# Kernel tuning notes

Measured on AMD Instinct MI355X. Metric: run time of the kernel, lower is better.

The kernel has to match this reference:

```python
import jax, jax.numpy as jnp
import numpy as np

L_MAX = 119
D_MODEL = 128
N_HEADS = 4
HEAD_DIM = 32


def _rope_tables():
    # matches torch: inv_freq over arange(0,128,2)/128, t=arange(119), cast to bf16
    channel_range = jnp.arange(0, D_MODEL, 2, dtype=jnp.float32)
    inv_freq = 1.0 / (10000.0 ** (channel_range / D_MODEL))
    t = jnp.arange(L_MAX, dtype=jnp.float32)
    freqs = jnp.outer(t, inv_freq)  # (119, 64)
    return jnp.cos(freqs).astype(jnp.bfloat16), jnp.sin(freqs).astype(jnp.bfloat16)


def _apply_rotary(x, cos, sin):
    # x: (b, l, 128); half-rotation on the full model dim (pre head-split)
    l = x.shape[1]
    d = x.shape[-1] // 2
    x1, x2 = x[..., :d], x[..., d:]
    c, s = cos[:l], sin[:l]
    y1 = x1 * c + x2 * s
    y2 = x1 * (-s) + x2 * c
    return jnp.concatenate([y1, y2], axis=-1).astype(x.dtype)


def setup_inputs() -> dict:
    key = jax.random.key(0)
    k1, k2, k3, k4, k5 = jax.random.split(key, 5)
    b, l = 2048, L_MAX
    return {
        "x": jax.random.normal(k1, (b, l, D_MODEL), dtype=jnp.float32),
        "W_qkv": jax.random.normal(k2, (3 * D_MODEL, D_MODEL), dtype=jnp.float32) * 0.05,
        "b_qkv": jax.random.normal(k3, (3 * D_MODEL,), dtype=jnp.float32) * 0.02,
        "W_fc2": jax.random.normal(k4, (D_MODEL, D_MODEL), dtype=jnp.float32) * 0.05,
        "b_fc2": jax.random.normal(k5, (D_MODEL,), dtype=jnp.float32) * 0.02,
    }


def reference(x, W_qkv, b_qkv, W_fc2, b_fc2):
    b, l, _ = x.shape
    cos, sin = _rope_tables()

    qkv = x @ W_qkv.T + b_qkv  # (b, l, 384)
    q, k, v = jnp.split(qkv, 3, axis=-1)
    q = _apply_rotary(q, cos, sin)
    k = _apply_rotary(k, cos, sin)

    # faithful to source: view(b, l, 32, 4) then 'b l d h -> b h l d'
    def split_heads(t):
        return t.reshape(b, l, HEAD_DIM, N_HEADS).transpose(0, 3, 1, 2)  # (b, h, l, d)

    q, k, v = split_heads(q), split_heads(k), split_heads(v)

    scale = 1.0 / np.sqrt(HEAD_DIM)
    scores = jnp.einsum("bhld,bhmd->bhlm", q, k) * scale  # (b, h, l, l)
    causal = jnp.tril(jnp.ones((l, l), dtype=bool))
    scores = jnp.where(causal, scores, jnp.float32(-jnp.inf))
    attn = jax.nn.softmax(scores, axis=-1)
    y = jnp.einsum("bhlm,bhmd->bhld", attn, v)  # (b, h, l, d)

    # faithful to source: transpose(1,2) then view(b, l, 128) -> layout h*32+d
    y = y.transpose(0, 2, 1, 3).reshape(b, l, D_MODEL)
    y = y @ W_fc2.T + b_fc2
    return jax.nn.silu(y)
```

## Files before the change

kernel.cpp:

```cpp
#include <hip/hip_runtime.h>
#include <hip/hip_bf16.h>
#include <math.h>


#define L_SEQ 119
#define D_MODEL 128
#define SCALE 0.17677669529663687f
#define NEGINF -1e30f

typedef __bf16 bf16x8 __attribute__((ext_vector_type(8)));
typedef __bf16 bf16x2 __attribute__((ext_vector_type(2)));
typedef float f32x4 __attribute__((ext_vector_type(4)));

__global__ void rope_tab_kernel(bf16x2* __restrict__ tabb) {
  int i = blockIdx.x * blockDim.x + threadIdx.x;
  if (i >= L_SEQ * 64) return;
  int l = i >> 6, j = i & 63;
  float inv = 1.0f / powf(10000.0f, (float)(2 * j) / 128.0f);
  float f = (float)l * inv;
  bf16x2 cs;
  cs[0] = (__bf16)cosf(f);
  cs[1] = (__bf16)sinf(f);
  tabb[i] = cs;
}

__global__ void wprep_kernel(const float* __restrict__ Wqkv,
                             const float* __restrict__ bqkv,
                             __bf16* __restrict__ Wb, float* __restrict__ bb) {
  int i = blockIdx.x * 256 + threadIdx.x;
  int j = i & 7, lane = (i >> 3) & 63, kb = (i >> 9) & 3, nt = i >> 11;
  int ln15 = lane & 15;
  int nch = nt * 16 + ln15;
  int h = nch / 96, rem = nch % 96, qkv = rem >> 5, d = rem & 31;
  int srow = qkv * 128 + d * 4 + h;
  int k = kb * 32 + (lane >> 4) * 8 + j;
  Wb[i] = (__bf16)Wqkv[srow * 128 + k];
  if (i < 384) {
    int h2 = i / 96, r2 = i % 96, q2 = r2 >> 5, d2 = r2 & 31;
    bb[i] = bqkv[q2 * 128 + d2 * 4 + h2];
  }
}

__global__ void wprep2_kernel(const float* __restrict__ Wfc2,
                              __bf16* __restrict__ Wf2b) {
  int i = blockIdx.x * 256 + threadIdx.x;
  int j = i & 7, lane = (i >> 3) & 63, kb = (i >> 9) & 3, nt = i >> 11;
  int n = nt * 16 + (lane & 15);
  int k = kb * 32 + (lane >> 4) * 8 + j;
  Wf2b[i] = (__bf16)Wfc2[n * 128 + k];
}

__global__ __launch_bounds__(512) void fused_all(
    const float* __restrict__ x, const __bf16* __restrict__ Wb,
    const float* __restrict__ bb, const bf16x2* __restrict__ tabb,
    const __bf16* __restrict__ Wf2b, const float* __restrict__ bfc2,
    float* __restrict__ out) {
  __shared__ __align__(16) __bf16 qs[2 * 119 * 34];
  __shared__ __align__(16) __bf16 ks[2 * 119 * 34];
  __shared__ __align__(16) __bf16 vT[2 * 32 * 128];

  const int t = threadIdx.x, b = blockIdx.x;
  const int lane = t & 63, wv = t >> 6;
  const int ln15 = lane & 15, kg = lane >> 4;
  const int ww = wv & 3, hh = wv >> 2;

  for (int i = t; i < 2 * 32 * 9; i += 512) {
    int hl = i / 288, rem = i % 288, rr = rem / 9, cc = L_SEQ + rem % 9;
    int vr = hl * 32 + rr;
    vT[vr * 128 + (cc ^ ((vr & 7) << 3))] = (__bf16)0.0f;
  }

  for (int g = 0; g < 2; ++g) {
    if (g) __syncthreads();

    bf16x8 af[2][4];
#pragma unroll
    for (int ms = 0; ms < 2; ++ms) {
      int xr = (ww + ms * 4) * 16 + ln15;
      if (xr > L_SEQ - 1) xr = L_SEQ - 1;
      const float* xrow = x + ((size_t)b * L_SEQ + xr) * 128;
#pragma unroll
      for (int kb = 0; kb < 4; ++kb) {
        float4 lo = *(const float4*)&xrow[kb * 32 + kg * 8];
        float4 hi = *(const float4*)&xrow[kb * 32 + kg * 8 + 4];
        bf16x8 v;
        v[0] = (__bf16)lo.x; v[1] = (__bf16)lo.y; v[2] = (__bf16)lo.z; v[3] = (__bf16)lo.w;
        v[4] = (__bf16)hi.x; v[5] = (__bf16)hi.y; v[6] = (__bf16)hi.z; v[7] = (__bf16)hi.w;
        af[ms][kb] = v;
      }
    }

    const int h = 2 * g + hh;
#pragma unroll
    for (int pair = 0; pair < 3; ++pair) {
      f32x4 acc[2][2] = {};
#pragma unroll
      for (int half = 0; half < 2; ++half) {
        const int nt = g * 12 + hh * 6 + pair * 2 + half;
        bf16x8 wf[4];
#pragma unroll
        for (int kb = 0; kb < 4; ++kb)
          wf[kb] = *(const bf16x8*)&Wb[(((nt * 4 + kb) * 64) + lane) * 8];
#pragma unroll
        for (int kb = 0; kb < 4; ++kb) {
          acc[0][half] = __builtin_amdgcn_mfma_f32_16x16x32_bf16(af[0][kb], wf[kb], acc[0][half], 0, 0, 0);
          acc[1][half] = __builtin_amdgcn_mfma_f32_16x16x32_bf16(af[1][kb], wf[kb], acc[1][half], 0, 0, 0);
        }
      }
      const float b0 = bb[(g * 12 + hh * 6 + pair * 2) * 16 + ln15];
      const float b1 = bb[(g * 12 + hh * 6 + pair * 2 + 1) * 16 + ln15];
#pragma unroll
      for (int ms = 0; ms < 2; ++ms) {
        const int mt = ww + ms * 4;
#pragma unroll
        for (int r = 0; r < 4; ++r) {
          int l = mt * 16 + kg * 4 + r;
          if (l < L_SEQ) {
            float v1 = acc[ms][0][r] + b0, v2 = acc[ms][1][r] + b1;
            if (pair < 2) {
              bf16x2 tcs = tabb[l * 64 + 4 * ln15 + h];
              float cs0 = (float)tcs[0], cs1 = (float)tcs[1];
              if (pair == 0) { v1 *= SCALE; v2 *= SCALE; }
              bf16x2 pk;
              pk[0] = (__bf16)(v1 * cs0 + v2 * cs1);
              pk[1] = (__bf16)(v2 * cs0 - v1 * cs1);
              __bf16* base = pair ? ks : qs;
              *(bf16x2*)&base[(hh * L_SEQ + l) * 34 + 2 * ln15] = pk;
            } else {
              int vr0 = hh * 32 + ln15, vr1 = vr0 + 16;
              vT[vr0 * 128 + (l ^ ((vr0 & 7) << 3))] = (__bf16)v1;
              vT[vr1 * 128 + (l ^ ((vr1 & 7) << 3))] = (__bf16)v2;
            }
          }
        }
      }
    }
    __syncthreads();

    const int srcLo = ln15 + ((kg & 1) << 5);
    const int srcHi = srcLo + 16;
#pragma unroll
    for (int ms = 0; ms < 2; ++ms) {
      const int m2 = ms ? (7 - ww) : ww;
      int qrow = m2 * 16 + ln15;
      if (qrow > L_SEQ - 1) qrow = L_SEQ - 1;
      bf16x8 qf = *(const bf16x8*)&qs[(hh * L_SEQ + qrow) * 34 + kg * 8];
      f32x4 s[8];
#pragma unroll
      for (int nt = 0; nt < 8; ++nt) {
        if (nt <= m2) {
          int krow = nt * 16 + ln15;
          if (krow > L_SEQ - 1) krow = L_SEQ - 1;
          bf16x8 kf = *(const bf16x8*)&ks[(hh * L_SEQ + krow) * 34 + kg * 8];
          f32x4 z = {};
          s[nt] = __builtin_amdgcn_mfma_f32_16x16x32_bf16(kf, qf, z, 0, 0, 0);
        }
      }
      float mx = NEGINF;
#pragma unroll
      for (int nt = 0; nt < 8; ++nt) {
        if (nt <= m2) {
          if (nt == m2) {
#pragma unroll
            for (int r = 0; r < 4; ++r)
              s[nt][r] = (kg * 4 + r <= ln15) ? s[nt][r] : NEGINF;
          }
#pragma unroll
          for (int r = 0; r < 4; ++r) mx = fmaxf(mx, s[nt][r]);
        }
      }
      mx = fmaxf(mx, __shfl_xor(mx, 16));
      mx = fmaxf(mx, __shfl_xor(mx, 32));
      float sum = 0.0f;
#pragma unroll
      for (int nt = 0; nt < 8; ++nt) {
        if (nt <= m2) {
#pragma unroll
          for (int r = 0; r < 4; ++r) { s[nt][r] = __expf(s[nt][r] - mx); sum += s[nt][r]; }
        }
      }
      sum += __shfl_xor(sum, 16);
      sum += __shfl_xor(sum, 32);
      float inv = 1.0f / sum;
      unsigned pk01[8], pk23[8];
#pragma unroll
      for (int nt = 0; nt < 8; ++nt) { pk01[nt] = 0u; pk23[nt] = 0u; }
#pragma unroll
      for (int nt = 0; nt < 8; ++nt) {
        if (nt <= m2) {
          union { bf16x2 v; unsigned u; } a, bcc;
          a.v[0] = (__bf16)s[nt][0]; a.v[1] = (__bf16)s[nt][1];
          bcc.v[0] = (__bf16)s[nt][2]; bcc.v[1] = (__bf16)s[nt][3];
          pk01[nt] = a.u; pk23[nt] = bcc.u;
        }
      }
      f32x4 o[2] = {};
#pragma unroll
      for (int kb = 0; kb < 4; ++kb) {
        if (kb <= (m2 >> 1)) {
          unsigned e0 = (unsigned)__shfl((int)pk01[2 * kb], srcLo);
          unsigned o0 = (unsigned)__shfl((int)pk01[2 * kb + 1], srcLo);
          unsigned e1 = (unsigned)__shfl((int)pk23[2 * kb], srcLo);
          unsigned o1 = (unsigned)__shfl((int)pk23[2 * kb + 1], srcLo);
          unsigned e2 = (unsigned)__shfl((int)pk01[2 * kb], srcHi);
          unsigned o2 = (unsigned)__shfl((int)pk01[2 * kb + 1], srcHi);
          unsigned e3 = (unsigned)__shfl((int)pk23[2 * kb], srcHi);
          unsigned o3 = (unsigned)__shfl((int)pk23[2 * kb + 1], srcHi);
          const bool odd = (kg & 2) != 0;
          union { unsigned w[4]; bf16x8 v; } A;
          A.w[0] = odd ? o0 : e0;
          A.w[1] = odd ? o1 : e1;
          A.w[2] = odd ? o2 : e2;
          A.w[3] = odd ? o3 : e3;
#pragma unroll
          for (int n2 = 0; n2 < 2; ++n2) {
            int vr = hh * 32 + n2 * 16 + ln15;
            bf16x8 vf = *(const bf16x8*)&vT[vr * 128 + ((kb * 32 + kg * 8) ^ ((vr & 7) << 3))];
            o[n2] = __builtin_amdgcn_mfma_f32_16x16x32_bf16(A.v, vf, o[n2], 0, 0, 0);
          }
        }
      }
      float invr[4];
#pragma unroll
      for (int r = 0; r < 4; ++r) invr[r] = __shfl(inv, kg * 4 + r);
#pragma unroll
      for (int n2 = 0; n2 < 2; ++n2)
#pragma unroll
        for (int r = 0; r < 4; ++r) {
          int l = m2 * 16 + kg * 4 + r;
          if (l < L_SEQ)
            out[((size_t)b * L_SEQ + l) * 128 + h * 32 + n2 * 16 + ln15] =
                o[n2][r] * invr[r];
        }
    }
  }

  __syncthreads();
  {
    int yr = wv * 16 + ln15;
    if (yr > L_SEQ - 1) yr = L_SEQ - 1;
    const float* yrow = out + ((size_t)b * L_SEQ + yr) * 128;
    bf16x8 af2[4];
#pragma unroll
    for (int kb = 0; kb < 4; ++kb) {
      float4 lo = *(const float4*)&yrow[kb * 32 + kg * 8];
      float4 hi = *(const float4*)&yrow[kb * 32 + kg * 8 + 4];
      bf16x8 v;
      v[0] = (__bf16)lo.x; v[1] = (__bf16)lo.y; v[2] = (__bf16)lo.z; v[3] = (__bf16)lo.w;
      v[4] = (__bf16)hi.x; v[5] = (__bf16)hi.y; v[6] = (__bf16)hi.z; v[7] = (__bf16)hi.w;
      af2[kb] = v;
    }
    float bc[8];
#pragma unroll
    for (int nt = 0; nt < 8; ++nt) bc[nt] = bfc2[nt * 16 + ln15];
    f32x4 acc2[8] = {};
#pragma unroll
    for (int nt = 0; nt < 8; ++nt)
#pragma unroll
      for (int kb = 0; kb < 4; ++kb)
        acc2[nt] = __builtin_amdgcn_mfma_f32_16x16x32_bf16(
            af2[kb], *(const bf16x8*)&Wf2b[(((nt * 4 + kb) * 64) + lane) * 8],
            acc2[nt], 0, 0, 0);
#pragma unroll
    for (int nt = 0; nt < 8; ++nt)
#pragma unroll
      for (int r = 0; r < 4; ++r) {
        int row = wv * 16 + kg * 4 + r, c = nt * 16 + ln15;
        if (row < L_SEQ) {
          float vv = acc2[nt][r] + bc[nt];
          out[((size_t)b * L_SEQ + row) * 128 + c] = vv / (1.0f + __expf(-vv));
        }
      }
  }
}

extern "C" void kernel_launch(void* const* d_in, const int* in_sizes, int n_in,
                              void* d_out, int out_size, void* d_ws,
                              size_t ws_size, hipStream_t stream) {
  const float* x = (const float*)d_in[0];
  const float* Wqkv = (const float*)d_in[1];
  const float* bqkv = (const float*)d_in[2];
  const float* Wfc2 = (const float*)d_in[3];
  const float* bfc2 = (const float*)d_in[4];
  float* out = (float*)d_out;

  char* ws = (char*)d_ws;
  bf16x2* tabb = (bf16x2*)ws;
  __bf16* Wb = (__bf16*)(ws + 30720);
  float* bb = (float*)(ws + 30720 + 98304);
  __bf16* Wf2b = (__bf16*)(ws + 30720 + 98304 + 1536);

  const int B = in_sizes[0] / (L_SEQ * D_MODEL);
  rope_tab_kernel<<<(L_SEQ * 64 + 255) / 256, 256, 0, stream>>>(tabb);
  wprep_kernel<<<192, 256, 0, stream>>>(Wqkv, bqkv, Wb, bb);
  wprep2_kernel<<<64, 256, 0, stream>>>(Wfc2, Wf2b);
  fused_all<<<B, 512, 0, stream>>>(x, Wb, bb, tabb, Wf2b, bfc2, out);
}
```

Baseline: 231.3 us.

## Switch QKV and attention to 32x32x16 MFMA tiles and process all heads at once

Rewrites the QKV projection and attention stages to use 32x32x16 bf16 MFMA tiles instead of 16x16x32. All four heads are now computed in a single pass rather than two sequential head groups, which removes one barrier and the repeated loading of x. The RoPE table is staged in padded shared memory, and Q/K rows are padded to 128. This raises the LDS footprint considerably (roughly 110KB), which can limit blocks per CU. It also increases register pressure from the 16-wide accumulators.

```diff
diff --git a/kernel.cpp b/kernel.cpp
--- a/kernel.cpp
+++ b/kernel.cpp
@@ -11,33 +11,32 @@
 typedef __bf16 bf16x8 __attribute__((ext_vector_type(8)));
 typedef __bf16 bf16x2 __attribute__((ext_vector_type(2)));
 typedef float f32x4 __attribute__((ext_vector_type(4)));
-
-__global__ void rope_tab_kernel(bf16x2* __restrict__ tabb) {
+typedef float f32x16 __attribute__((ext_vector_type(16)));
+
+__global__ void rope_tab_kernel(unsigned* __restrict__ tabu) {
   int i = blockIdx.x * blockDim.x + threadIdx.x;
   if (i >= L_SEQ * 64) return;
   int l = i >> 6, j = i & 63;
   float inv = 1.0f / powf(10000.0f, (float)(2 * j) / 128.0f);
   float f = (float)l * inv;
-  bf16x2 cs;
-  cs[0] = (__bf16)cosf(f);
-  cs[1] = (__bf16)sinf(f);
-  tabb[i] = cs;
+  union { bf16x2 v; unsigned u; } cs;
+  cs.v[0] = (__bf16)cosf(f);
+  cs.v[1] = (__bf16)sinf(f);
+  tabu[i] = cs.u;
 }
 
 __global__ void wprep_kernel(const float* __restrict__ Wqkv,
                              const float* __restrict__ bqkv,
-                             __bf16* __restrict__ Wb, float* __restrict__ bb) {
+                             __bf16* __restrict__ Wb, float* __restrict__ bb2) {
   int i = blockIdx.x * 256 + threadIdx.x;
-  int j = i & 7, lane = (i >> 3) & 63, kb = (i >> 9) & 3, nt = i >> 11;
-  int ln15 = lane & 15;
-  int nch = nt * 16 + ln15;
-  int h = nch / 96, rem = nch % 96, qkv = rem >> 5, d = rem & 31;
-  int srow = qkv * 128 + d * 4 + h;
-  int k = kb * 32 + (lane >> 4) * 8 + j;
-  Wb[i] = (__bf16)Wqkv[srow * 128 + k];
+  int j = i & 7, lane = (i >> 3) & 63, ks = (i >> 9) & 7, nt = i >> 12;
+  int d = lane & 31;
+  int h = nt / 3, qkv = nt % 3;
+  int k = ks * 16 + (lane >> 5) * 8 + j;
+  Wb[i] = (__bf16)Wqkv[(qkv * 128 + d * 4 + h) * 128 + k];
   if (i < 384) {
-    int h2 = i / 96, r2 = i % 96, q2 = r2 >> 5, d2 = r2 & 31;
-    bb[i] = bqkv[q2 * 128 + d2 * 4 + h2];
+    int nt2 = i >> 5, dd = i & 31;
+    bb2[i] = bqkv[(nt2 % 3) * 128 + dd * 4 + (nt2 / 3)];
   }
 }
 
@@ -52,191 +51,188 @@
 
 __global__ __launch_bounds__(512) void fused_all(
     const float* __restrict__ x, const __bf16* __restrict__ Wb,
-    const float* __restrict__ bb, const bf16x2* __restrict__ tabb,
+    const float* __restrict__ bb2, const unsigned* __restrict__ tabu,
     const __bf16* __restrict__ Wf2b, const float* __restrict__ bfc2,
     float* __restrict__ out) {
-  __shared__ __align__(16) __bf16 qs[2 * 119 * 34];
-  __shared__ __align__(16) __bf16 ks[2 * 119 * 34];
-  __shared__ __align__(16) __bf16 vT[2 * 32 * 128];
+  __shared__ __align__(16) __bf16 qs[4 * 128 * 40];
+  __shared__ __align__(16) __bf16 ksm[4 * 128 * 40];
+  __shared__ __align__(16) __bf16 vT[4 * 32 * 128];
+  __shared__ unsigned tabL[L_SEQ * 65];
 
   const int t = threadIdx.x, b = blockIdx.x;
   const int lane = t & 63, wv = t >> 6;
-  const int ln15 = lane & 15, kg = lane >> 4;
-  const int ww = wv & 3, hh = wv >> 2;
-
-  for (int i = t; i < 2 * 32 * 9; i += 512) {
-    int hl = i / 288, rem = i % 288, rr = rem / 9, cc = L_SEQ + rem % 9;
-    int vr = hl * 32 + rr;
-    vT[vr * 128 + (cc ^ ((vr & 7) << 3))] = (__bf16)0.0f;
-  }
-
-  for (int g = 0; g < 2; ++g) {
-    if (g) __syncthreads();
-
-    bf16x8 af[2][4];
-#pragma unroll
-    for (int ms = 0; ms < 2; ++ms) {
-      int xr = (ww + ms * 4) * 16 + ln15;
-      if (xr > L_SEQ - 1) xr = L_SEQ - 1;
-      const float* xrow = x + ((size_t)b * L_SEQ + xr) * 128;
-#pragma unroll
-      for (int kb = 0; kb < 4; ++kb) {
-        float4 lo = *(const float4*)&xrow[kb * 32 + kg * 8];
-        float4 hi = *(const float4*)&xrow[kb * 32 + kg * 8 + 4];
-        bf16x8 v;
-        v[0] = (__bf16)lo.x; v[1] = (__bf16)lo.y; v[2] = (__bf16)lo.z; v[3] = (__bf16)lo.w;
-        v[4] = (__bf16)hi.x; v[5] = (__bf16)hi.y; v[6] = (__bf16)hi.z; v[7] = (__bf16)hi.w;
-        af[ms][kb] = v;
-      }
-    }
-
-    const int h = 2 * g + hh;
-#pragma unroll
-    for (int pair = 0; pair < 3; ++pair) {
-      f32x4 acc[2][2] = {};
-#pragma unroll
-      for (int half = 0; half < 2; ++half) {
-        const int nt = g * 12 + hh * 6 + pair * 2 + half;
-        bf16x8 wf[4];
-#pragma unroll
-        for (int kb = 0; kb < 4; ++kb)
-          wf[kb] = *(const bf16x8*)&Wb[(((nt * 4 + kb) * 64) + lane) * 8];
-#pragma unroll
-        for (int kb = 0; kb < 4; ++kb) {
-          acc[0][half] = __builtin_amdgcn_mfma_f32_16x16x32_bf16(af[0][kb], wf[kb], acc[0][half], 0, 0, 0);
-          acc[1][half] = __builtin_amdgcn_mfma_f32_16x16x32_bf16(af[1][kb], wf[kb], acc[1][half], 0, 0, 0);
-        }
-      }
-      const float b0 = bb[(g * 12 + hh * 6 + pair * 2) * 16 + ln15];
-      const float b1 = bb[(g * 12 + hh * 6 + pair * 2 + 1) * 16 + ln15];
-#pragma unroll
-      for (int ms = 0; ms < 2; ++ms) {
-        const int mt = ww + ms * 4;
-#pragma unroll
-        for (int r = 0; r < 4; ++r) {
-          int l = mt * 16 + kg * 4 + r;
-          if (l < L_SEQ) {
-            float v1 = acc[ms][0][r] + b0, v2 = acc[ms][1][r] + b1;
-            if (pair < 2) {
-              bf16x2 tcs = tabb[l * 64 + 4 * ln15 + h];
-              float cs0 = (float)tcs[0], cs1 = (float)tcs[1];
-              if (pair == 0) { v1 *= SCALE; v2 *= SCALE; }
-              bf16x2 pk;
-              pk[0] = (__bf16)(v1 * cs0 + v2 * cs1);
-              pk[1] = (__bf16)(v2 * cs0 - v1 * cs1);
-              __bf16* base = pair ? ks : qs;
-              *(bf16x2*)&base[(hh * L_SEQ + l) * 34 + 2 * ln15] = pk;
-            } else {
-              int vr0 = hh * 32 + ln15, vr1 = vr0 + 16;
-              vT[vr0 * 128 + (l ^ ((vr0 & 7) << 3))] = (__bf16)v1;
-              vT[vr1 * 128 + (l ^ ((vr1 & 7) << 3))] = (__bf16)v2;
+  const int ln31 = lane & 31, hi = lane >> 5;
+
+  for (int i = t; i < L_SEQ * 64; i += 512)
+    tabL[(i >> 6) * 65 + (i & 63)] = tabu[i];
+  for (int i = t; i < 4 * 32 * 9; i += 512) {
+    int hd = i / 9, cc = L_SEQ + i % 9, d = hd & 31;
+    vT[hd * 128 + (cc ^ ((d & 7) << 3))] = (__bf16)0.0f;
+  }
+  __syncthreads();
+
+  const int mt = wv & 3, g2 = wv >> 2;
+  const int l_me = mt * 32 + ln31;
+  const bool live = (l_me < L_SEQ);
+  {
+    int xr = live ? l_me : (L_SEQ - 1);
+    const float* xrow = x + ((size_t)b * L_SEQ + xr) * 128;
+    bf16x8 af[8];
+#pragma unroll
+    for (int ks = 0; ks < 8; ++ks) {
+      float4 lo = *(const float4*)&xrow[ks * 16 + hi * 8];
+      float4 hi4 = *(const float4*)&xrow[ks * 16 + hi * 8 + 4];
+      bf16x8 v;
+      v[0] = (__bf16)lo.x; v[1] = (__bf16)lo.y; v[2] = (__bf16)lo.z; v[3] = (__bf16)lo.w;
+      v[4] = (__bf16)hi4.x; v[5] = (__bf16)hi4.y; v[6] = (__bf16)hi4.z; v[7] = (__bf16)hi4.w;
+      af[ks] = v;
+    }
+#pragma unroll
+    for (int r = 0; r < 3; ++r) {
+      const int nt0 = g2 * 6 + 2 * r, nt1 = nt0 + 1;
+      f32x16 a0 = {}, a1 = {};
+#pragma unroll
+      for (int ks = 0; ks < 8; ++ks) {
+        bf16x8 wf0 = *(const bf16x8*)&Wb[(((nt0 * 8 + ks) * 64) + lane) * 8];
+        bf16x8 wf1 = *(const bf16x8*)&Wb[(((nt1 * 8 + ks) * 64) + lane) * 8];
+        a0 = __builtin_amdgcn_mfma_f32_32x32x16_bf16(wf0, af[ks], a0, 0, 0, 0);
+        a1 = __builtin_amdgcn_mfma_f32_32x32x16_bf16(wf1, af[ks], a1, 0, 0, 0);
+      }
+#pragma unroll
+      for (int e = 0; e < 2; ++e) {
+        const int nt = e ? nt1 : nt0;
+        const f32x16& A = e ? a1 : a0;
+        const int h = nt / 3, qkv = nt % 3;
+        if (qkv < 2) {
+          __bf16* base = (qkv == 0) ? qs : ksm;
+          if (live) {
+#pragma unroll
+            for (int rg = 0; rg < 8; ++rg) {
+              const int c_lo = (rg & 3) + 8 * (rg >> 2);
+              int d = c_lo + 4 * hi;
+              union { bf16x2 v; unsigned u; } cs;
+              cs.u = tabL[l_me * 65 + 4 * d + h];
+              float c = (float)cs.v[0], s = (float)cs.v[1];
+              float v1 = A[rg] + bb2[nt * 32 + d];
+              float v2 = A[rg + 8] + bb2[nt * 32 + d + 16];
+              if (qkv == 0) { v1 *= SCALE; v2 *= SCALE; }
+              union { bf16x2 v; unsigned u; } pk;
+              pk.v[0] = (__bf16)(v1 * c + v2 * s);
+              pk.v[1] = (__bf16)(v2 * c - v1 * s);
+              *(unsigned*)&base[(h * 128 + l_me) * 40 + 2 * d] = pk.u;
             }
           }
-        }
-      }
-    }
-    __syncthreads();
-
-    const int srcLo = ln15 + ((kg & 1) << 5);
-    const int srcHi = srcLo + 16;
-#pragma unroll
-    for (int ms = 0; ms < 2; ++ms) {
-      const int m2 = ms ? (7 - ww) : ww;
-      int qrow = m2 * 16 + ln15;
-      if (qrow > L_SEQ - 1) qrow = L_SEQ - 1;
-      bf16x8 qf = *(const bf16x8*)&qs[(hh * L_SEQ + qrow) * 34 + kg * 8];
-      f32x4 s[8];
-#pragma unroll
-      for (int nt = 0; nt < 8; ++nt) {
-        if (nt <= m2) {
-          int krow = nt * 16 + ln15;
-          if (krow > L_SEQ - 1) krow = L_SEQ - 1;
-          bf16x8 kf = *(const bf16x8*)&ks[(hh * L_SEQ + krow) * 34 + kg * 8];
-          f32x4 z = {};
-          s[nt] = __builtin_amdgcn_mfma_f32_16x16x32_bf16(kf, qf, z, 0, 0, 0);
+        } else {
+          if (live) {
+#pragma unroll
+            for (int rg = 0; rg < 16; ++rg) {
+              const int d = (rg & 3) + 8 * (rg >> 2) + 4 * hi;
+              float val = A[rg] + bb2[nt * 32 + d];
+              vT[(h * 32 + d) * 128 + (l_me ^ ((d & 7) << 3))] = (__bf16)val;
+            }
+          }
+        }
+      }
+    }
+  }
+  __syncthreads();
+
+  {
+    const int h = wv >> 1;
+#pragma unroll
+    for (int ts = 0; ts < 2; ++ts) {
+      const int qt = ts ? (3 - (wv & 1)) : (wv & 1);
+      bf16x8 qf0 = *(const bf16x8*)&qs[(h * 128 + qt * 32 + ln31) * 40 + hi * 8];
+      bf16x8 qf1 = *(const bf16x8*)&qs[(h * 128 + qt * 32 + ln31) * 40 + 16 + hi * 8];
+      f32x16 s[4];
+#pragma unroll
+      for (int kt = 0; kt < 4; ++kt) {
+        if (kt <= qt) {
+          bf16x8 kf0 = *(const bf16x8*)&ksm[(h * 128 + kt * 32 + ln31) * 40 + hi * 8];
+          bf16x8 kf1 = *(const bf16x8*)&ksm[(h * 128 + kt * 32 + ln31) * 40 + 16 + hi * 8];
+          f32x16 z = {};
+          z = __builtin_amdgcn_mfma_f32_32x32x16_bf16(kf0, qf0, z, 0, 0, 0);
+          s[kt] = __builtin_amdgcn_mfma_f32_32x32x16_bf16(kf1, qf1, z, 0, 0, 0);
+        }
+      }
+      {
+#pragma unroll
+        for (int rg = 0; rg < 16; ++rg) {
+          const int c_lo = (rg & 3) + 8 * (rg >> 2);
+#pragma unroll
+          for (int kt = 0; kt < 4; ++kt) {
+            if (kt == qt) {
+              int crow = c_lo + 4 * hi;
+              s[kt][rg] = (crow <= ln31) ? s[kt][rg] : NEGINF;
+            }
+          }
         }
       }
       float mx = NEGINF;
 #pragma unroll
-      for (int nt = 0; nt < 8; ++nt) {
-        if (nt <= m2) {
-          if (nt == m2) {
-#pragma unroll
-            for (int r = 0; r < 4; ++r)
-              s[nt][r] = (kg * 4 + r <= ln15) ? s[nt][r] : NEGINF;
-          }
-#pragma unroll
-          for (int r = 0; r < 4; ++r) mx = fmaxf(mx, s[nt][r]);
-        }
-      }
-      mx = fmaxf(mx, __shfl_xor(mx, 16));
+      for (int kt = 0; kt < 4; ++kt)
+        if (kt <= qt)
+#pragma unroll
+          for (int rg = 0; rg < 16; ++rg) mx = fmaxf(mx, s[kt][rg]);
       mx = fmaxf(mx, __shfl_xor(mx, 32));
       float sum = 0.0f;
 #pragma unroll
-      for (int nt = 0; nt < 8; ++nt) {
-        if (nt <= m2) {
-#pragma unroll
-          for (int r = 0; r < 4; ++r) { s[nt][r] = __expf(s[nt][r] - mx); sum += s[nt][r]; }
-        }
-      }
-      sum += __shfl_xor(sum, 16);
+      for (int kt = 0; kt < 4; ++kt)
+        if (kt <= qt)
+#pragma unroll
+          for (int rg = 0; rg < 16; ++rg) {
+            s[kt][rg] = __expf(s[kt][rg] - mx);
+            sum += s[kt][rg];
+          }
       sum += __shfl_xor(sum, 32);
       float inv = 1.0f / sum;
-      unsigned pk01[8], pk23[8];
-#pragma unroll
-      for (int nt = 0; nt < 8; ++nt) { pk01[nt] = 0u; pk23[nt] = 0u; }
-#pragma unroll
-      for (int nt = 0; nt < 8; ++nt) {
-        if (nt <= m2) {
-          union { bf16x2 v; unsigned u; } a, bcc;
-          a.v[0] = (__bf16)s[nt][0]; a.v[1] = (__bf16)s[nt][1];
-          bcc.v[0] = (__bf16)s[nt][2]; bcc.v[1] = (__bf16)s[nt][3];
-          pk01[nt] = a.u; pk23[nt] = bcc.u;
-        }
-      }
-      f32x4 o[2] = {};
-#pragma unroll
-      for (int kb = 0; kb < 4; ++kb) {
-        if (kb <= (m2 >> 1)) {
-          unsigned e0 = (unsigned)__shfl((int)pk01[2 * kb], srcLo);
-          unsigned o0 = (unsigned)__shfl((int)pk01[2 * kb + 1], srcLo);
-          unsigned e1 = (unsigned)__shfl((int)pk23[2 * kb], srcLo);
-          unsigned o1 = (unsigned)__shfl((int)pk23[2 * kb + 1], srcLo);
-          unsigned e2 = (unsigned)__shfl((int)pk01[2 * kb], srcHi);
-          unsigned o2 = (unsigned)__shfl((int)pk01[2 * kb + 1], srcHi);
-          unsigned e3 = (unsigned)__shfl((int)pk23[2 * kb], srcHi);
-          unsigned o3 = (unsigned)__shfl((int)pk23[2 * kb + 1], srcHi);
-          const bool odd = (kg & 2) != 0;
-          union { unsigned w[4]; bf16x8 v; } A;
-          A.w[0] = odd ? o0 : e0;
-          A.w[1] = odd ? o1 : e1;
-          A.w[2] = odd ? o2 : e2;
-          A.w[3] = odd ? o3 : e3;
-#pragma unroll
-          for (int n2 = 0; n2 < 2; ++n2) {
-            int vr = hh * 32 + n2 * 16 + ln15;
-            bf16x8 vf = *(const bf16x8*)&vT[vr * 128 + ((kb * 32 + kg * 8) ^ ((vr & 7) << 3))];
-            o[n2] = __builtin_amdgcn_mfma_f32_16x16x32_bf16(A.v, vf, o[n2], 0, 0, 0);
-          }
-        }
-      }
-      float invr[4];
-#pragma unroll
-      for (int r = 0; r < 4; ++r) invr[r] = __shfl(inv, kg * 4 + r);
-#pragma unroll
-      for (int n2 = 0; n2 < 2; ++n2)
-#pragma unroll
-        for (int r = 0; r < 4; ++r) {
-          int l = m2 * 16 + kg * 4 + r;
-          if (l < L_SEQ)
-            out[((size_t)b * L_SEQ + l) * 128 + h * 32 + n2 * 16 + ln15] =
-                o[n2][r] * invr[r];
-        }
+      unsigned pk[4][8];
+#pragma unroll
+      for (int kt = 0; kt < 4; ++kt) {
+        if (kt <= qt) {
+#pragma unroll
+          for (int p = 0; p < 8; ++p) {
+            union { bf16x2 v; unsigned u; } w;
+            w.v[0] = (__bf16)(s[kt][2 * p] * inv);
+            w.v[1] = (__bf16)(s[kt][2 * p + 1] * inv);
+            pk[kt][p] = w.u;
+          }
+        }
+      }
+      f32x16 o = {};
+#pragma unroll
+      for (int kt = 0; kt < 4; ++kt) {
+        if (kt <= qt) {
+#pragma unroll
+          for (int m = 0; m < 2; ++m) {
+            unsigned f0 = (unsigned)__shfl_xor((int)pk[kt][4 * m + 0], 32);
+            unsigned f1 = (unsigned)__shfl_xor((int)pk[kt][4 * m + 1], 32);
+            unsigned f2 = (unsigned)__shfl_xor((int)pk[kt][4 * m + 2], 32);
+            unsigned f3 = (unsigned)__shfl_xor((int)pk[kt][4 * m + 3], 32);
+            union { unsigned w[4]; bf16x8 v; } Aw;
+            Aw.w[0] = hi ? f2 : pk[kt][4 * m + 0];
+            Aw.w[1] = hi ? f3 : pk[kt][4 * m + 1];
+            Aw.w[2] = hi ? pk[kt][4 * m + 2] : f0;
+            Aw.w[3] = hi ? pk[kt][4 * m + 3] : f1;
+            bf16x8 vf = *(const bf16x8*)&vT[(h * 32 + ln31) * 128 +
+                ((kt * 32 + m * 16 + hi * 8) ^ ((ln31 & 7) << 3))];
+            o = __builtin_amdgcn_mfma_f32_32x32x16_bf16(Aw.v, vf, o, 0, 0, 0);
+          }
+        }
+      }
+#pragma unroll
+      for (int rg = 0; rg < 16; ++rg) {
+        const int c_lo = (rg & 3) + 8 * (rg >> 2);
+        int l = qt * 32 + c_lo + 4 * hi;
+        if (l < L_SEQ)
+          out[((size_t)b * L_SEQ + l) * 128 + h * 32 + ln31] = o[rg];
+      }
     }
   }
 
   __syncthreads();
   {
+    const int ln15 = lane & 15, kg = lane >> 4;
     int yr = wv * 16 + ln15;
     if (yr > L_SEQ - 1) yr = L_SEQ - 1;
     const float* yrow = out + ((size_t)b * L_SEQ + yr) * 128;
@@ -244,10 +240,10 @@
 #pragma unroll
     for (int kb = 0; kb < 4; ++kb) {
       float4 lo = *(const float4*)&yrow[kb * 32 + kg * 8];
-      float4 hi = *(const float4*)&yrow[kb * 32 + kg * 8 + 4];
+      float4 hi4 = *(const float4*)&yrow[kb * 32 + kg * 8 + 4];
       bf16x8 v;
       v[0] = (__bf16)lo.x; v[1] = (__bf16)lo.y; v[2] = (__bf16)lo.z; v[3] = (__bf16)lo.w;
-      v[4] = (__bf16)hi.x; v[5] = (__bf16)hi.y; v[6] = (__bf16)hi.z; v[7] = (__bf16)hi.w;
+      v[4] = (__bf16)hi4.x; v[5] = (__bf16)hi4.y; v[6] = (__bf16)hi4.z; v[7] = (__bf16)hi4.w;
       af2[kb] = v;
     }
     float bc[8];
@@ -285,14 +281,14 @@
   float* out = (float*)d_out;
 
   char* ws = (char*)d_ws;
-  bf16x2* tabb = (bf16x2*)ws;
+  unsigned* tabu = (unsigned*)ws;
   __bf16* Wb = (__bf16*)(ws + 30720);
-  float* bb = (float*)(ws + 30720 + 98304);
+  float* bb2 = (float*)(ws + 30720 + 98304);
   __bf16* Wf2b = (__bf16*)(ws + 30720 + 98304 + 1536);
 
   const int B = in_sizes[0] / (L_SEQ * D_MODEL);
-  rope_tab_kernel<<<(L_SEQ * 64 + 255) / 256, 256, 0, stream>>>(tabb);
-  wprep_kernel<<<192, 256, 0, stream>>>(Wqkv, bqkv, Wb, bb);
+  rope_tab_kernel<<<(L_SEQ * 64 + 255) / 256, 256, 0, stream>>>(tabu);
+  wprep_kernel<<<192, 256, 0, stream>>>(Wqkv, bqkv, Wb, bb2);
   wprep2_kernel<<<64, 256, 0, stream>>>(Wfc2, Wf2b);
-  fused_all<<<B, 512, 0, stream>>>(x, Wb, bb, tabb, Wf2b, bfc2, out);
-}
+  fused_all<<<B, 512, 0, stream>>>(x, Wb, bb2, tabu, Wf2b, bfc2, out);
+}
```

After: 221.8 us. -4.1%, faster.
